# Kernel optimization log

Measured on AMD Instinct MI355X. Metric: run time of the kernel, lower is better.

## Reference

```python
import jax, jax.numpy as jnp
import numpy as np


def setup_inputs() -> dict:
    key = jax.random.key(0)
    k0, k1, k2, k3 = jax.random.split(key, 4)
    T, H, I, E = 2048, 2048, 5632, 8
    return {
        "hidden_states": jax.random.normal(k0, (T, H), dtype=jnp.float32),
        "gate_w": jax.random.normal(k1, (E, H), dtype=jnp.float32) * 0.02,
        "w1": jax.random.normal(k2, (E, 2 * I, H), dtype=jnp.float32) * 0.02,
        "w2": jax.random.normal(k3, (E, H, I), dtype=jnp.float32) * 0.02,
        "top_k": 2,
    }


def reference(hidden_states, gate_w, w1, w2, top_k):
    # hidden_states: [T, H]; gate_w: [E, H]; w1: [E, 2I, H]; w2: [E, H, I]
    T = hidden_states.shape[0]
    E = w1.shape[0]
    router_logits = hidden_states @ gate_w.T                    # [T, E]
    probs = jax.nn.softmax(router_logits, axis=-1)
    topk_w, topk_idx = jax.lax.top_k(probs, top_k)              # [T, k]
    # renormalize=False in fused_moe: use raw softmax top-k weights.
    # Dense combine matrix C[t, e] = weight of expert e for token t (0 if unrouted).
    combine = jnp.zeros((T, E), dtype=probs.dtype)
    combine = combine.at[jnp.arange(T)[:, None], topk_idx].add(topk_w)
    out = jnp.zeros_like(hidden_states)
    for e in range(E):  # small fixed expert loop
        gate_up = hidden_states @ w1[e].T                       # [T, 2I]
        g, u = jnp.split(gate_up, 2, axis=-1)
        h = jax.nn.silu(g) * u                                  # SiluAndMul
        out = out + combine[:, e:e + 1] * (h @ w2[e].T)         # [T, H]
    return out
```

## Files before the change

kernel.cpp:

```cpp
#include <hip/hip_runtime.h>
#include <hip/hip_bf16.h>

typedef __bf16 bf16_t;
typedef __bf16 bf16x8 __attribute__((ext_vector_type(8)));
typedef float  f32x4  __attribute__((ext_vector_type(4)));

constexpr int T_ = 2048, H_ = 2048, I_ = 5632, E_ = 8, S_ = T_ * 2;

constexpr size_t OFF_HB    = 0;
constexpr size_t OFF_HOUT  = OFF_HB    + (size_t)T_ * H_ * 2;
constexpr size_t OFF_DPART = OFF_HOUT  + (size_t)S_ * I_ * 2;
constexpr size_t OFF_TOS   = OFF_DPART + (size_t)S_ * H_ * 4;
constexpr size_t OFF_SOT   = OFF_TOS   + (size_t)S_ * 4;
constexpr size_t OFF_TKI   = OFF_SOT   + (size_t)S_ * 4;
constexpr size_t OFF_TKW   = OFF_TKI   + (size_t)S_ * 4;
constexpr size_t OFF_CNT   = OFF_TKW   + (size_t)S_ * 4;
constexpr size_t OFF_OFFS  = OFF_CNT   + 64;
constexpr size_t OFF_CUR   = OFF_OFFS  + 64;

__device__ __forceinline__ void gload16(const void* g, void* l) {
  __builtin_amdgcn_global_load_lds(
      (const __attribute__((address_space(1))) void*)g,
      (__attribute__((address_space(3))) void*)l, 16, 0, 0);
}

__device__ __forceinline__ bf16x8 cvt8(f32x4 a, f32x4 b) {
  bf16x8 r;
  r[0]=(bf16_t)a[0]; r[1]=(bf16_t)a[1]; r[2]=(bf16_t)a[2]; r[3]=(bf16_t)a[3];
  r[4]=(bf16_t)b[0]; r[5]=(bf16_t)b[1]; r[6]=(bf16_t)b[2]; r[7]=(bf16_t)b[3];
  return r;
}

__global__ __launch_bounds__(256)
void router_kernel(const float* __restrict__ hs, const float* __restrict__ gw,
                   int* __restrict__ tki, float* __restrict__ tkw,
                   int* __restrict__ counts, bf16_t* __restrict__ hb)
{
  const int t = blockIdx.x;
  const int tid = threadIdx.x;
  const int lane = tid & 63, wid = tid >> 6;
  const float* hrow = hs + (size_t)t * H_;
  const int c0 = tid * 8;
  float4 h0 = *(const float4*)(hrow + c0);
  float4 h1 = *(const float4*)(hrow + c0 + 4);
  bf16x8 hv;
  hv[0]=(bf16_t)h0.x; hv[1]=(bf16_t)h0.y; hv[2]=(bf16_t)h0.z; hv[3]=(bf16_t)h0.w;
  hv[4]=(bf16_t)h1.x; hv[5]=(bf16_t)h1.y; hv[6]=(bf16_t)h1.z; hv[7]=(bf16_t)h1.w;
  *(bf16x8*)(hb + (size_t)t * H_ + c0) = hv;

  float acc[E_];
  #pragma unroll
  for (int e = 0; e < E_; ++e) {
    const float* g = gw + (size_t)e * H_ + c0;
    float4 g0 = *(const float4*)(g);
    float4 g1 = *(const float4*)(g + 4);
    acc[e] = h0.x*g0.x + h0.y*g0.y + h0.z*g0.z + h0.w*g0.w
           + h1.x*g1.x + h1.y*g1.y + h1.z*g1.z + h1.w*g1.w;
  }
  #pragma unroll
  for (int e = 0; e < E_; ++e)
    #pragma unroll
    for (int o = 32; o > 0; o >>= 1)
      acc[e] += __shfl_down(acc[e], o);
  __shared__ float red[4][E_];
  if (lane == 0)
    #pragma unroll
    for (int e = 0; e < E_; ++e) red[wid][e] = acc[e];
  __syncthreads();
  if (tid == 0) {
    float l[E_];
    #pragma unroll
    for (int e = 0; e < E_; ++e) l[e] = red[0][e] + red[1][e] + red[2][e] + red[3][e];
    float m = l[0];
    #pragma unroll
    for (int e = 1; e < E_; ++e) m = fmaxf(m, l[e]);
    float p[E_]; float s = 0.f;
    #pragma unroll
    for (int e = 0; e < E_; ++e) { p[e] = __expf(l[e] - m); s += p[e]; }
    int i1 = 0;
    #pragma unroll
    for (int e = 1; e < E_; ++e) if (l[e] > l[i1]) i1 = e;
    int i2 = (i1 == 0) ? 1 : 0;
    #pragma unroll
    for (int e = 0; e < E_; ++e) if (e != i1 && l[e] > l[i2]) i2 = e;
    tki[2*t] = i1; tki[2*t+1] = i2;
    tkw[2*t] = p[i1] / s; tkw[2*t+1] = p[i2] / s;
    atomicAdd(&counts[i1], 1);
    atomicAdd(&counts[i2], 1);
  }
}

__global__ void scan_kernel(const int* __restrict__ counts, const int* __restrict__ tki,
                            int* __restrict__ offs, int* __restrict__ cursor,
                            int* __restrict__ tos, int* __restrict__ sot)
{
  if (threadIdx.x == 0) {
    int run = 0;
    for (int e = 0; e < E_; ++e) { offs[e] = run; cursor[e] = run; run += counts[e]; }
  }
  __syncthreads();
  for (int t = threadIdx.x; t < T_; t += blockDim.x) {
    #pragma unroll
    for (int k = 0; k < 2; ++k) {
      int e = tki[2*t + k];
      int s = atomicAdd(&cursor[e], 1);
      tos[s] = t;
      sot[2*t + k] = s;
    }
  }
}

constexpr int G1_BM = 128, G1_BN = 64, G1_BK = 32;
constexpr int G1_BUF = 8192 + 16384;

__global__ __launch_bounds__(256, 3)
void gemm1_kernel(const bf16_t* __restrict__ hb, const float* __restrict__ w1,
                  const int* __restrict__ tos, const int* __restrict__ offs,
                  const int* __restrict__ counts, bf16_t* __restrict__ hout)
{
  const int bid = blockIdx.x;
  const int e   = bid & 7;
  const int idx = bid >> 3;
  const int mt  = idx & 15;
  const int nt  = idx >> 4;

  const int cnt = counts[e];
  const int m0 = mt * G1_BM;
  if (m0 >= cnt) return;
  const int off = offs[e];
  const int n0 = nt * G1_BN;

  const float* Wg = w1 + (size_t)e * (2 * (size_t)I_ * H_) + (size_t)n0 * H_;

  __shared__ char smem[2 * G1_BUF];

  const int tid = threadIdx.x;
  const int lane = tid & 63, wid = tid >> 6;
  const int wm = wid >> 1, wn = wid & 1;
  const int l15 = lane & 15, l4 = lane >> 4;

  const bf16_t* agp[2]; int aoff[2];
  #pragma unroll
  for (int i = 0; i < 2; ++i) {
    int q = wid * 2 + i;
    int rp = q * 8 + (lane >> 3);
    int w  = (lane & 7) ^ (rp & 7);
    int row = 2 * rp + (w >> 2);
    int slot = off + m0 + row, mx = off + cnt - 1;
    if (slot > mx) slot = mx;
    agp[i]  = hb + (size_t)tos[slot] * H_ + (w & 3) * 8;
    aoff[i] = q * 1024;
  }
  const float* bgp[4]; int boff[4];
  #pragma unroll
  for (int i = 0; i < 4; ++i) {
    int q = wid * 4 + i;
    int row = q * 8 + (lane >> 3);
    int w   = (lane & 7) ^ (row & 7);
    size_t wr = (row < 64) ? (size_t)row : (size_t)(I_ - 64 + row);
    bgp[i]  = Wg + wr * H_ + w * 4;
    boff[i] = q * 1024;
  }

  auto stage = [&](int b, int t) {
    char* ab = smem + b * G1_BUF;
    char* bb = ab + 8192;
    const int k0 = t * G1_BK;
    #pragma unroll
    for (int i = 0; i < 2; ++i) gload16(agp[i] + k0, ab + aoff[i]);
    #pragma unroll
    for (int i = 0; i < 4; ++i) gload16(bgp[i] + k0, bb + boff[i]);
  };

  f32x4 accg[4][2], accu[4][2];
  #pragma unroll
  for (int mi = 0; mi < 4; ++mi)
    #pragma unroll
    for (int ni = 0; ni < 2; ++ni) {
      accg[mi][ni] = f32x4{0.f,0.f,0.f,0.f};
      accu[mi][ni] = f32x4{0.f,0.f,0.f,0.f};
    }

  const int physA = ((((l15 & 1) << 2) | l4) ^ ((l15 >> 1) & 7)) * 16;
  const int aro   = (l15 >> 1);
  const int pB0   = (((2 * l4) ^ (l15 & 7))) * 16;

  auto compute = [&](int b) {
    const char* ab = smem + b * G1_BUF;
    const char* bb = ab + 8192;
    bf16x8 af[4], bgf[2], buf2[2];
    #pragma unroll
    for (int mi = 0; mi < 4; ++mi) {
      int rp = wm * 32 + mi * 8 + aro;
      af[mi] = *(const bf16x8*)(ab + rp * 128 + physA);
    }
    #pragma unroll
    for (int ni = 0; ni < 2; ++ni) {
      int rg = wn * 32 + ni * 16 + l15;
      const char* rowg = bb + rg * 128;
      const char* rowu = bb + (rg + 64) * 128;
      f32x4 g0 = *(const f32x4*)(rowg + pB0);
      f32x4 g1 = *(const f32x4*)(rowg + (pB0 ^ 16));
      f32x4 u0 = *(const f32x4*)(rowu + pB0);
      f32x4 u1 = *(const f32x4*)(rowu + (pB0 ^ 16));
      bgf[ni]  = cvt8(g0, g1);
      buf2[ni] = cvt8(u0, u1);
    }
    #pragma unroll
    for (int mi = 0; mi < 4; ++mi)
      #pragma unroll
      for (int ni = 0; ni < 2; ++ni) {
        accg[mi][ni] = __builtin_amdgcn_mfma_f32_16x16x32_bf16(af[mi], bgf[ni],  accg[mi][ni], 0, 0, 0);
        accu[mi][ni] = __builtin_amdgcn_mfma_f32_16x16x32_bf16(af[mi], buf2[ni], accu[mi][ni], 0, 0, 0);
      }
  };

  constexpr int NK = H_ / G1_BK;
  stage(0, 0);
  __syncthreads();
  int cur = 0;
  for (int t = 0; t < NK; ++t) {
    if (t + 1 < NK) stage(cur ^ 1, t + 1);
    compute(cur);
    __syncthreads();
    cur ^= 1;
  }

  #pragma unroll
  for (int mi = 0; mi < 4; ++mi)
    #pragma unroll
    for (int ni = 0; ni < 2; ++ni)
      #pragma unroll
      for (int j = 0; j < 4; ++j) {
        int rel = wm*64 + mi*16 + l4*4 + j;
        if (m0 + rel < cnt) {
          int col = n0 + wn*32 + ni*16 + l15;
          float g = accg[mi][ni][j];
          float u = accu[mi][ni][j];
          float hvv = (g / (1.0f + __expf(-g))) * u;
          hout[(size_t)(off + m0 + rel) * I_ + col] = (bf16_t)hvv;
        }
      }
}

constexpr int G2_BM = 128, G2_BN = 128, G2_BK = 32;
constexpr int G2_BUF = 8192 + 16384;

__global__ __launch_bounds__(256, 3)
void gemm2_kernel(const bf16_t* __restrict__ hbuf, const float* __restrict__ w2,
                  const int* __restrict__ offs, const int* __restrict__ counts,
                  float* __restrict__ dpart)
{
  const int bid = blockIdx.x;
  const int e   = bid & 7;
  const int idx = bid >> 3;
  const int mt  = idx & 15;
  const int nt  = idx >> 4;

  const int cnt = counts[e];
  const int m0 = mt * G2_BM;
  if (m0 >= cnt) return;
  const int off = offs[e];
  const int n0 = nt * G2_BN;
  const float* W = w2 + (size_t)e * ((size_t)H_ * I_) + (size_t)n0 * I_;

  __shared__ char smem[2 * G2_BUF];

  const int tid = threadIdx.x;
  const int lane = tid & 63, wid = tid >> 6;
  const int wm = wid >> 1, wn = wid & 1;
  const int l15 = lane & 15, l4 = lane >> 4;

  const bf16_t* agp[2]; int aoff[2];
  #pragma unroll
  for (int i = 0; i < 2; ++i) {
    int q = wid * 2 + i;
    int rp = q * 8 + (lane >> 3);
    int w  = (lane & 7) ^ (rp & 7);
    int row = 2 * rp + (w >> 2);
    int slot = off + m0 + row, mx = off + cnt - 1;
    if (slot > mx) slot = mx;
    agp[i]  = hbuf + (size_t)slot * I_ + (w & 3) * 8;
    aoff[i] = q * 1024;
  }
  const float* bgp[4]; int boff[4];
  #pragma unroll
  for (int i = 0; i < 4; ++i) {
    int q = wid * 4 + i;
    int row = q * 8 + (lane >> 3);
    int w   = (lane & 7) ^ (row & 7);
    bgp[i]  = W + (size_t)row * I_ + w * 4;
    boff[i] = q * 1024;
  }

  auto stage = [&](int b, int t) {
    char* ab = smem + b * G2_BUF;
    char* bb = ab + 8192;
    const int k0 = t * G2_BK;
    #pragma unroll
    for (int i = 0; i < 2; ++i) gload16(agp[i] + k0, ab + aoff[i]);
    #pragma unroll
    for (int i = 0; i < 4; ++i) gload16(bgp[i] + k0, bb + boff[i]);
  };

  f32x4 acc[4][4];
  #pragma unroll
  for (int mi = 0; mi < 4; ++mi)
    #pragma unroll
    for (int ni = 0; ni < 4; ++ni) acc[mi][ni] = f32x4{0.f,0.f,0.f,0.f};

  const int physA = ((((l15 & 1) << 2) | l4) ^ ((l15 >> 1) & 7)) * 16;
  const int aro   = (l15 >> 1);
  const int pB0   = (((2 * l4) ^ (l15 & 7))) * 16;

  auto compute = [&](int b) {
    const char* ab = smem + b * G2_BUF;
    const char* bb = ab + 8192;
    bf16x8 af[4], bf[4];
    #pragma unroll
    for (int mi = 0; mi < 4; ++mi) {
      int rp = wm * 32 + mi * 8 + aro;
      af[mi] = *(const bf16x8*)(ab + rp * 128 + physA);
    }
    #pragma unroll
    for (int ni = 0; ni < 4; ++ni) {
      int r = wn * 64 + ni * 16 + l15;
      const char* rowb = bb + r * 128;
      f32x4 b0 = *(const f32x4*)(rowb + pB0);
      f32x4 b1 = *(const f32x4*)(rowb + (pB0 ^ 16));
      bf[ni] = cvt8(b0, b1);
    }
    #pragma unroll
    for (int mi = 0; mi < 4; ++mi)
      #pragma unroll
      for (int ni = 0; ni < 4; ++ni)
        acc[mi][ni] = __builtin_amdgcn_mfma_f32_16x16x32_bf16(af[mi], bf[ni], acc[mi][ni], 0, 0, 0);
  };

  constexpr int NK = I_ / G2_BK;
  stage(0, 0);
  __syncthreads();
  int cur = 0;
  for (int t = 0; t < NK; ++t) {
    if (t + 1 < NK) stage(cur ^ 1, t + 1);
    compute(cur);
    __syncthreads();
    cur ^= 1;
  }

  #pragma unroll
  for (int mi = 0; mi < 4; ++mi)
    #pragma unroll
    for (int ni = 0; ni < 4; ++ni)
      #pragma unroll
      for (int j = 0; j < 4; ++j) {
        int rel = wm*64 + mi*16 + l4*4 + j;
        if (m0 + rel < cnt) {
          int col = n0 + wn*64 + ni*16 + l15;
          dpart[(size_t)(off + m0 + rel) * H_ + col] = acc[mi][ni][j];
        }
      }
}

__global__ __launch_bounds__(256)
void combine_kernel(const float* __restrict__ dpart, const int* __restrict__ sot,
                    const float* __restrict__ tkw, float* __restrict__ out)
{
  int idx = blockIdx.x * 256 + threadIdx.x;
  int t = idx >> 9;
  int c = (idx & 511) * 4;
  float wA = tkw[2*t], wB = tkw[2*t+1];
  int sA = sot[2*t], sB = sot[2*t+1];
  float4 a = *(const float4*)(dpart + (size_t)sA * H_ + c);
  float4 b = *(const float4*)(dpart + (size_t)sB * H_ + c);
  float4 o;
  o.x = wA*a.x + wB*b.x; o.y = wA*a.y + wB*b.y;
  o.z = wA*a.z + wB*b.z; o.w = wA*a.w + wB*b.w;
  *(float4*)(out + (size_t)t * H_ + c) = o;
}

extern "C" void kernel_launch(void* const* d_in, const int* in_sizes, int n_in,
                              void* d_out, int out_size, void* d_ws, size_t ws_size,
                              hipStream_t stream) {
  const float* hs = (const float*)d_in[0];
  const float* gw = (const float*)d_in[1];
  const float* w1 = (const float*)d_in[2];
  const float* w2 = (const float*)d_in[3];
  float* out = (float*)d_out;
  char* ws = (char*)d_ws;

  bf16_t* hb    = (bf16_t*)(ws + OFF_HB);
  bf16_t* hout  = (bf16_t*)(ws + OFF_HOUT);
  float*  dpart = (float*) (ws + OFF_DPART);
  int*    tos   = (int*)   (ws + OFF_TOS);
  int*    sot   = (int*)   (ws + OFF_SOT);
  int*    tki   = (int*)   (ws + OFF_TKI);
  float*  tkw   = (float*) (ws + OFF_TKW);
  int*    cnt   = (int*)   (ws + OFF_CNT);
  int*    offp  = (int*)   (ws + OFF_OFFS);
  int*    curp  = (int*)   (ws + OFF_CUR);

  hipMemsetAsync(ws + OFF_CNT, 0, 64, stream);

  router_kernel<<<T_, 256, 0, stream>>>(hs, gw, tki, tkw, cnt, hb);
  scan_kernel<<<1, 256, 0, stream>>>(cnt, tki, offp, curp, tos, sot);
  gemm1_kernel<<<(T_ / G1_BM) * (I_ / G1_BN) * E_, 256, 0, stream>>>(hb, w1, tos, offp, cnt, hout);
  gemm2_kernel<<<(T_ / G2_BM) * (H_ / G2_BN) * E_, 256, 0, stream>>>(hout, w2, offp, cnt, dpart);
  combine_kernel<<<(T_ * H_ / 4) / 256, 256, 0, stream>>>(dpart, sot, tkw, out);
}
```

Baseline: 905.2 us.

## Retile expert GEMMs to 256-row tiles with 512-thread blocks

Both expert GEMM kernels move from 256-thread blocks with 128-row tiles to 512-thread blocks (8 waves) with 256-row M tiles. Each fp32 weight tile loaded from HBM is therefore reused across twice as many tokens. gemm2's N tile shrinks from 128 to 64, and the swizzle and staging index math is rewritten to match. This cuts weight re-reads, which dominate traffic since the weights are fp32. The cost is fewer, larger blocks, lower occupancy (2 blocks per CU), and more wasted rows on partially filled expert tiles.

```diff
diff --git a/kernel.cpp b/kernel.cpp
--- a/kernel.cpp
+++ b/kernel.cpp
@@ -110,10 +110,9 @@
   }
 }
 
-constexpr int G1_BM = 128, G1_BN = 64, G1_BK = 32;
-constexpr int G1_BUF = 8192 + 16384;
-
-__global__ __launch_bounds__(256, 3)
+constexpr int G1_BUF = 32768;
+
+__global__ __launch_bounds__(512, 2)
 void gemm1_kernel(const bf16_t* __restrict__ hb, const float* __restrict__ w1,
                   const int* __restrict__ tos, const int* __restrict__ offs,
                   const int* __restrict__ counts, bf16_t* __restrict__ hout)
@@ -121,14 +120,14 @@
   const int bid = blockIdx.x;
   const int e   = bid & 7;
   const int idx = bid >> 3;
-  const int mt  = idx & 15;
-  const int nt  = idx >> 4;
+  const int mt  = idx & 7;
+  const int nt  = idx >> 3;
 
   const int cnt = counts[e];
-  const int m0 = mt * G1_BM;
+  const int m0 = mt * 256;
   if (m0 >= cnt) return;
   const int off = offs[e];
-  const int n0 = nt * G1_BN;
+  const int n0 = nt * 64;
 
   const float* Wg = w1 + (size_t)e * (2 * (size_t)I_ * H_) + (size_t)n0 * H_;
 
@@ -143,20 +142,19 @@
   #pragma unroll
   for (int i = 0; i < 2; ++i) {
     int q = wid * 2 + i;
-    int rp = q * 8 + (lane >> 3);
-    int w  = (lane & 7) ^ (rp & 7);
-    int row = 2 * rp + (w >> 2);
+    int w = (lane & 7) ^ (lane >> 3);
+    int row = 2 * (q * 8 + (lane >> 3)) + (w >> 2);
     int slot = off + m0 + row, mx = off + cnt - 1;
     if (slot > mx) slot = mx;
     agp[i]  = hb + (size_t)tos[slot] * H_ + (w & 3) * 8;
     aoff[i] = q * 1024;
   }
-  const float* bgp[4]; int boff[4];
-  #pragma unroll
-  for (int i = 0; i < 4; ++i) {
-    int q = wid * 4 + i;
+  const float* bgp[2]; int boff[2];
+  #pragma unroll
+  for (int i = 0; i < 2; ++i) {
+    int q = wid * 2 + i;
     int row = q * 8 + (lane >> 3);
-    int w   = (lane & 7) ^ (row & 7);
+    int w   = (lane & 7) ^ (lane >> 3);
     size_t wr = (row < 64) ? (size_t)row : (size_t)(I_ - 64 + row);
     bgp[i]  = Wg + wr * H_ + w * 4;
     boff[i] = q * 1024;
@@ -164,12 +162,12 @@
 
   auto stage = [&](int b, int t) {
     char* ab = smem + b * G1_BUF;
-    char* bb = ab + 8192;
-    const int k0 = t * G1_BK;
+    char* bb = ab + 16384;
+    const int k0 = t * 32;
     #pragma unroll
     for (int i = 0; i < 2; ++i) gload16(agp[i] + k0, ab + aoff[i]);
     #pragma unroll
-    for (int i = 0; i < 4; ++i) gload16(bgp[i] + k0, bb + boff[i]);
+    for (int i = 0; i < 2; ++i) gload16(bgp[i] + k0, bb + boff[i]);
   };
 
   f32x4 accg[4][2], accu[4][2];
@@ -182,16 +180,15 @@
     }
 
   const int physA = ((((l15 & 1) << 2) | l4) ^ ((l15 >> 1) & 7)) * 16;
-  const int aro   = (l15 >> 1);
-  const int pB0   = (((2 * l4) ^ (l15 & 7))) * 16;
+  const int pB0   = ((2 * l4) ^ (l15 & 7)) * 16;
 
   auto compute = [&](int b) {
     const char* ab = smem + b * G1_BUF;
-    const char* bb = ab + 8192;
+    const char* bb = ab + 16384;
     bf16x8 af[4], bgf[2], buf2[2];
     #pragma unroll
     for (int mi = 0; mi < 4; ++mi) {
-      int rp = wm * 32 + mi * 8 + aro;
+      int rp = wm * 32 + mi * 8 + (l15 >> 1);
       af[mi] = *(const bf16x8*)(ab + rp * 128 + physA);
     }
     #pragma unroll
@@ -215,7 +212,7 @@
       }
   };
 
-  constexpr int NK = H_ / G1_BK;
+  constexpr int NK = H_ / 32;
   stage(0, 0);
   __syncthreads();
   int cur = 0;
@@ -243,10 +240,9 @@
       }
 }
 
-constexpr int G2_BM = 128, G2_BN = 128, G2_BK = 32;
-constexpr int G2_BUF = 8192 + 16384;
-
-__global__ __launch_bounds__(256, 3)
+constexpr int G2_BUF = 24576;
+
+__global__ __launch_bounds__(512, 2)
 void gemm2_kernel(const bf16_t* __restrict__ hbuf, const float* __restrict__ w2,
                   const int* __restrict__ offs, const int* __restrict__ counts,
                   float* __restrict__ dpart)
@@ -254,14 +250,14 @@
   const int bid = blockIdx.x;
   const int e   = bid & 7;
   const int idx = bid >> 3;
-  const int mt  = idx & 15;
-  const int nt  = idx >> 4;
+  const int mt  = idx & 7;
+  const int nt  = idx >> 3;
 
   const int cnt = counts[e];
-  const int m0 = mt * G2_BM;
+  const int m0 = mt * 256;
   if (m0 >= cnt) return;
   const int off = offs[e];
-  const int n0 = nt * G2_BN;
+  const int n0 = nt * 64;
   const float* W = w2 + (size_t)e * ((size_t)H_ * I_) + (size_t)n0 * I_;
 
   __shared__ char smem[2 * G2_BUF];
@@ -275,56 +271,47 @@
   #pragma unroll
   for (int i = 0; i < 2; ++i) {
     int q = wid * 2 + i;
-    int rp = q * 8 + (lane >> 3);
-    int w  = (lane & 7) ^ (rp & 7);
-    int row = 2 * rp + (w >> 2);
+    int w = (lane & 7) ^ (lane >> 3);
+    int row = 2 * (q * 8 + (lane >> 3)) + (w >> 2);
     int slot = off + m0 + row, mx = off + cnt - 1;
     if (slot > mx) slot = mx;
     agp[i]  = hbuf + (size_t)slot * I_ + (w & 3) * 8;
     aoff[i] = q * 1024;
   }
-  const float* bgp[4]; int boff[4];
-  #pragma unroll
-  for (int i = 0; i < 4; ++i) {
-    int q = wid * 4 + i;
-    int row = q * 8 + (lane >> 3);
-    int w   = (lane & 7) ^ (row & 7);
-    bgp[i]  = W + (size_t)row * I_ + w * 4;
-    boff[i] = q * 1024;
-  }
+  int w_ = (lane & 7) ^ (lane >> 3);
+  const float* bgp = W + (size_t)(wid * 8 + (lane >> 3)) * I_ + w_ * 4;
+  const int boff = wid * 1024;
 
   auto stage = [&](int b, int t) {
     char* ab = smem + b * G2_BUF;
-    char* bb = ab + 8192;
-    const int k0 = t * G2_BK;
+    char* bb = ab + 16384;
+    const int k0 = t * 32;
     #pragma unroll
     for (int i = 0; i < 2; ++i) gload16(agp[i] + k0, ab + aoff[i]);
-    #pragma unroll
-    for (int i = 0; i < 4; ++i) gload16(bgp[i] + k0, bb + boff[i]);
+    gload16(bgp + k0, bb + boff);
   };
 
-  f32x4 acc[4][4];
+  f32x4 acc[4][2];
   #pragma unroll
   for (int mi = 0; mi < 4; ++mi)
     #pragma unroll
-    for (int ni = 0; ni < 4; ++ni) acc[mi][ni] = f32x4{0.f,0.f,0.f,0.f};
+    for (int ni = 0; ni < 2; ++ni) acc[mi][ni] = f32x4{0.f,0.f,0.f,0.f};
 
   const int physA = ((((l15 & 1) << 2) | l4) ^ ((l15 >> 1) & 7)) * 16;
-  const int aro   = (l15 >> 1);
-  const int pB0   = (((2 * l4) ^ (l15 & 7))) * 16;
+  const int pB0   = ((2 * l4) ^ (l15 & 7)) * 16;
 
   auto compute = [&](int b) {
     const char* ab = smem + b * G2_BUF;
-    const char* bb = ab + 8192;
-    bf16x8 af[4], bf[4];
+    const char* bb = ab + 16384;
+    bf16x8 af[4], bf[2];
     #pragma unroll
     for (int mi = 0; mi < 4; ++mi) {
-      int rp = wm * 32 + mi * 8 + aro;
+      int rp = wm * 32 + mi * 8 + (l15 >> 1);
       af[mi] = *(const bf16x8*)(ab + rp * 128 + physA);
     }
     #pragma unroll
-    for (int ni = 0; ni < 4; ++ni) {
-      int r = wn * 64 + ni * 16 + l15;
+    for (int ni = 0; ni < 2; ++ni) {
+      int r = wn * 32 + ni * 16 + l15;
       const char* rowb = bb + r * 128;
       f32x4 b0 = *(const f32x4*)(rowb + pB0);
       f32x4 b1 = *(const f32x4*)(rowb + (pB0 ^ 16));
@@ -333,11 +320,11 @@
     #pragma unroll
     for (int mi = 0; mi < 4; ++mi)
       #pragma unroll
-      for (int ni = 0; ni < 4; ++ni)
+      for (int ni = 0; ni < 2; ++ni)
         acc[mi][ni] = __builtin_amdgcn_mfma_f32_16x16x32_bf16(af[mi], bf[ni], acc[mi][ni], 0, 0, 0);
   };
 
-  constexpr int NK = I_ / G2_BK;
+  constexpr int NK = I_ / 32;
   stage(0, 0);
   __syncthreads();
   int cur = 0;
@@ -351,12 +338,12 @@
   #pragma unroll
   for (int mi = 0; mi < 4; ++mi)
     #pragma unroll
-    for (int ni = 0; ni < 4; ++ni)
+    for (int ni = 0; ni < 2; ++ni)
       #pragma unroll
       for (int j = 0; j < 4; ++j) {
         int rel = wm*64 + mi*16 + l4*4 + j;
         if (m0 + rel < cnt) {
-          int col = n0 + wn*64 + ni*16 + l15;
+          int col = n0 + wn*32 + ni*16 + l15;
           dpart[(size_t)(off + m0 + rel) * H_ + col] = acc[mi][ni][j];
         }
       }
@@ -404,7 +391,7 @@
 
   router_kernel<<<T_, 256, 0, stream>>>(hs, gw, tki, tkw, cnt, hb);
   scan_kernel<<<1, 256, 0, stream>>>(cnt, tki, offp, curp, tos, sot);
-  gemm1_kernel<<<(T_ / G1_BM) * (I_ / G1_BN) * E_, 256, 0, stream>>>(hb, w1, tos, offp, cnt, hout);
-  gemm2_kernel<<<(T_ / G2_BM) * (H_ / G2_BN) * E_, 256, 0, stream>>>(hout, w2, offp, cnt, dpart);
+  gemm1_kernel<<<8 * (2 * I_ / 128) * E_, 512, 0, stream>>>(hb, w1, tos, offp, cnt, hout);
+  gemm2_kernel<<<8 * (H_ / 64) * E_, 512, 0, stream>>>(hout, w2, offp, cnt, dpart);
   combine_kernel<<<(T_ * H_ / 4) / 256, 256, 0, stream>>>(dpart, sot, tkw, out);
 }
```

Result: slower. 1.128 ms (+24.6%).

## Load fp32 weight fragments directly to registers, bypassing LDS for B operand

Applied to the files above, without the earlier changes.

Both expert GEMMs stop staging the fp32 weight tile through shared memory. Each lane now reads its MFMA B fragment straight from global memory into registers one step ahead and converts it to bf16 after the MFMAs run. Only the bf16 activation tile stays in LDS, using a smaller 64-byte-row swizzle. This cuts the LDS footprint and LDS traffic, which may allow higher occupancy, but weight reuse across the two M-waves now depends on the cache and each lane issues more global loads.

```diff
diff --git a/kernel.cpp b/kernel.cpp
--- a/kernel.cpp
+++ b/kernel.cpp
@@ -110,8 +110,7 @@
   }
 }
 
-constexpr int G1_BM = 128, G1_BN = 64, G1_BK = 32;
-constexpr int G1_BUF = 8192 + 16384;
+constexpr int G1_BUF = 8192;
 
 __global__ __launch_bounds__(256, 3)
 void gemm1_kernel(const bf16_t* __restrict__ hb, const float* __restrict__ w1,
@@ -125,10 +124,10 @@
   const int nt  = idx >> 4;
 
   const int cnt = counts[e];
-  const int m0 = mt * G1_BM;
+  const int m0 = mt * 128;
   if (m0 >= cnt) return;
   const int off = offs[e];
-  const int n0 = nt * G1_BN;
+  const int n0 = nt * 64;
 
   const float* Wg = w1 + (size_t)e * (2 * (size_t)I_ * H_) + (size_t)n0 * H_;
 
@@ -143,33 +142,35 @@
   #pragma unroll
   for (int i = 0; i < 2; ++i) {
     int q = wid * 2 + i;
-    int rp = q * 8 + (lane >> 3);
-    int w  = (lane & 7) ^ (rp & 7);
-    int row = 2 * rp + (w >> 2);
-    int slot = off + m0 + row, mx = off + cnt - 1;
+    int R = q * 16 + (lane >> 2);
+    int wanted = (lane & 3) ^ ((lane >> 2) & 3);
+    int slot = off + m0 + R, mx = off + cnt - 1;
     if (slot > mx) slot = mx;
-    agp[i]  = hb + (size_t)tos[slot] * H_ + (w & 3) * 8;
+    agp[i]  = hb + (size_t)tos[slot] * H_ + wanted * 8;
     aoff[i] = q * 1024;
   }
-  const float* bgp[4]; int boff[4];
-  #pragma unroll
-  for (int i = 0; i < 4; ++i) {
-    int q = wid * 4 + i;
-    int row = q * 8 + (lane >> 3);
-    int w   = (lane & 7) ^ (row & 7);
-    size_t wr = (row < 64) ? (size_t)row : (size_t)(I_ - 64 + row);
-    bgp[i]  = Wg + wr * H_ + w * 4;
-    boff[i] = q * 1024;
-  }
-
-  auto stage = [&](int b, int t) {
+  auto stageA = [&](int b, int t) {
     char* ab = smem + b * G1_BUF;
-    char* bb = ab + 8192;
-    const int k0 = t * G1_BK;
-    #pragma unroll
-    for (int i = 0; i < 2; ++i) gload16(agp[i] + k0, ab + aoff[i]);
-    #pragma unroll
-    for (int i = 0; i < 4; ++i) gload16(bgp[i] + k0, bb + boff[i]);
+    #pragma unroll
+    for (int i = 0; i < 2; ++i) gload16(agp[i] + t * 32, ab + aoff[i]);
+  };
+
+  const float* bp00 = Wg + (size_t)(wn * 32 +  0 + l15) * H_ + l4 * 8;
+  const float* bp01 = Wg + (size_t)(wn * 32 + 16 + l15) * H_ + l4 * 8;
+  const float* bp10 = bp00 + (size_t)I_ * H_;
+  const float* bp11 = bp01 + (size_t)I_ * H_;
+
+  f32x4 br0, br1, br2, br3, br4, br5, br6, br7;
+  auto loadB = [&](int k0) {
+    br0 = *(const f32x4*)(bp00 + k0); br1 = *(const f32x4*)(bp00 + k0 + 4);
+    br2 = *(const f32x4*)(bp01 + k0); br3 = *(const f32x4*)(bp01 + k0 + 4);
+    br4 = *(const f32x4*)(bp10 + k0); br5 = *(const f32x4*)(bp10 + k0 + 4);
+    br6 = *(const f32x4*)(bp11 + k0); br7 = *(const f32x4*)(bp11 + k0 + 4);
+  };
+  bf16x8 bgf0, bgf1, buf0, buf1;
+  auto cvtB = [&]() {
+    bgf0 = cvt8(br0, br1); bgf1 = cvt8(br2, br3);
+    buf0 = cvt8(br4, br5); buf1 = cvt8(br6, br7);
   };
 
   f32x4 accg[4][2], accu[4][2];
@@ -181,47 +182,33 @@
       accu[mi][ni] = f32x4{0.f,0.f,0.f,0.f};
     }
 
-  const int physA = ((((l15 & 1) << 2) | l4) ^ ((l15 >> 1) & 7)) * 16;
-  const int aro   = (l15 >> 1);
-  const int pB0   = (((2 * l4) ^ (l15 & 7))) * 16;
-
+  const int achunk = (l4 ^ (l15 & 3)) * 16;
   auto compute = [&](int b) {
     const char* ab = smem + b * G1_BUF;
-    const char* bb = ab + 8192;
-    bf16x8 af[4], bgf[2], buf2[2];
+    bf16x8 af[4];
     #pragma unroll
     for (int mi = 0; mi < 4; ++mi) {
-      int rp = wm * 32 + mi * 8 + aro;
-      af[mi] = *(const bf16x8*)(ab + rp * 128 + physA);
-    }
-    #pragma unroll
-    for (int ni = 0; ni < 2; ++ni) {
-      int rg = wn * 32 + ni * 16 + l15;
-      const char* rowg = bb + rg * 128;
-      const char* rowu = bb + (rg + 64) * 128;
-      f32x4 g0 = *(const f32x4*)(rowg + pB0);
-      f32x4 g1 = *(const f32x4*)(rowg + (pB0 ^ 16));
-      f32x4 u0 = *(const f32x4*)(rowu + pB0);
-      f32x4 u1 = *(const f32x4*)(rowu + (pB0 ^ 16));
-      bgf[ni]  = cvt8(g0, g1);
-      buf2[ni] = cvt8(u0, u1);
-    }
-    #pragma unroll
-    for (int mi = 0; mi < 4; ++mi)
-      #pragma unroll
-      for (int ni = 0; ni < 2; ++ni) {
-        accg[mi][ni] = __builtin_amdgcn_mfma_f32_16x16x32_bf16(af[mi], bgf[ni],  accg[mi][ni], 0, 0, 0);
-        accu[mi][ni] = __builtin_amdgcn_mfma_f32_16x16x32_bf16(af[mi], buf2[ni], accu[mi][ni], 0, 0, 0);
-      }
-  };
-
-  constexpr int NK = H_ / G1_BK;
-  stage(0, 0);
+      int R = wm * 64 + mi * 16 + l15;
+      af[mi] = *(const bf16x8*)(ab + R * 64 + achunk);
+    }
+    #pragma unroll
+    for (int mi = 0; mi < 4; ++mi) {
+      accg[mi][0] = __builtin_amdgcn_mfma_f32_16x16x32_bf16(af[mi], bgf0, accg[mi][0], 0, 0, 0);
+      accg[mi][1] = __builtin_amdgcn_mfma_f32_16x16x32_bf16(af[mi], bgf1, accg[mi][1], 0, 0, 0);
+      accu[mi][0] = __builtin_amdgcn_mfma_f32_16x16x32_bf16(af[mi], buf0, accu[mi][0], 0, 0, 0);
+      accu[mi][1] = __builtin_amdgcn_mfma_f32_16x16x32_bf16(af[mi], buf1, accu[mi][1], 0, 0, 0);
+    }
+  };
+
+  constexpr int NK = H_ / 32;
+  loadB(0); stageA(0, 0);
+  cvtB();
   __syncthreads();
   int cur = 0;
   for (int t = 0; t < NK; ++t) {
-    if (t + 1 < NK) stage(cur ^ 1, t + 1);
+    if (t + 1 < NK) { loadB((t + 1) * 32); stageA(cur ^ 1, t + 1); }
     compute(cur);
+    if (t + 1 < NK) cvtB();
     __syncthreads();
     cur ^= 1;
   }
@@ -243,8 +230,7 @@
       }
 }
 
-constexpr int G2_BM = 128, G2_BN = 128, G2_BK = 32;
-constexpr int G2_BUF = 8192 + 16384;
+constexpr int G2_BUF = 8192;
 
 __global__ __launch_bounds__(256, 3)
 void gemm2_kernel(const bf16_t* __restrict__ hbuf, const float* __restrict__ w2,
@@ -258,10 +244,10 @@
   const int nt  = idx >> 4;
 
   const int cnt = counts[e];
-  const int m0 = mt * G2_BM;
+  const int m0 = mt * 128;
   if (m0 >= cnt) return;
   const int off = offs[e];
-  const int n0 = nt * G2_BN;
+  const int n0 = nt * 128;
   const float* W = w2 + (size_t)e * ((size_t)H_ * I_) + (size_t)n0 * I_;
 
   __shared__ char smem[2 * G2_BUF];
@@ -275,32 +261,35 @@
   #pragma unroll
   for (int i = 0; i < 2; ++i) {
     int q = wid * 2 + i;
-    int rp = q * 8 + (lane >> 3);
-    int w  = (lane & 7) ^ (rp & 7);
-    int row = 2 * rp + (w >> 2);
-    int slot = off + m0 + row, mx = off + cnt - 1;
+    int R = q * 16 + (lane >> 2);
+    int wanted = (lane & 3) ^ ((lane >> 2) & 3);
+    int slot = off + m0 + R, mx = off + cnt - 1;
     if (slot > mx) slot = mx;
-    agp[i]  = hbuf + (size_t)slot * I_ + (w & 3) * 8;
+    agp[i]  = hbuf + (size_t)slot * I_ + wanted * 8;
     aoff[i] = q * 1024;
   }
-  const float* bgp[4]; int boff[4];
-  #pragma unroll
-  for (int i = 0; i < 4; ++i) {
-    int q = wid * 4 + i;
-    int row = q * 8 + (lane >> 3);
-    int w   = (lane & 7) ^ (row & 7);
-    bgp[i]  = W + (size_t)row * I_ + w * 4;
-    boff[i] = q * 1024;
-  }
-
-  auto stage = [&](int b, int t) {
+  auto stageA = [&](int b, int t) {
     char* ab = smem + b * G2_BUF;
-    char* bb = ab + 8192;
-    const int k0 = t * G2_BK;
-    #pragma unroll
-    for (int i = 0; i < 2; ++i) gload16(agp[i] + k0, ab + aoff[i]);
-    #pragma unroll
-    for (int i = 0; i < 4; ++i) gload16(bgp[i] + k0, bb + boff[i]);
+    #pragma unroll
+    for (int i = 0; i < 2; ++i) gload16(agp[i] + t * 32, ab + aoff[i]);
+  };
+
+  const float* bp0 = W + (size_t)(wn * 64 +  0 + l15) * I_ + l4 * 8;
+  const float* bp1 = W + (size_t)(wn * 64 + 16 + l15) * I_ + l4 * 8;
+  const float* bp2 = W + (size_t)(wn * 64 + 32 + l15) * I_ + l4 * 8;
+  const float* bp3 = W + (size_t)(wn * 64 + 48 + l15) * I_ + l4 * 8;
+
+  f32x4 br0, br1, br2, br3, br4, br5, br6, br7;
+  auto loadB = [&](int k0) {
+    br0 = *(const f32x4*)(bp0 + k0); br1 = *(const f32x4*)(bp0 + k0 + 4);
+    br2 = *(const f32x4*)(bp1 + k0); br3 = *(const f32x4*)(bp1 + k0 + 4);
+    br4 = *(const f32x4*)(bp2 + k0); br5 = *(const f32x4*)(bp2 + k0 + 4);
+    br6 = *(const f32x4*)(bp3 + k0); br7 = *(const f32x4*)(bp3 + k0 + 4);
+  };
+  bf16x8 bf0, bf1, bf2, bf3;
+  auto cvtB = [&]() {
+    bf0 = cvt8(br0, br1); bf1 = cvt8(br2, br3);
+    bf2 = cvt8(br4, br5); bf3 = cvt8(br6, br7);
   };
 
   f32x4 acc[4][4];
@@ -309,41 +298,33 @@
     #pragma unroll
     for (int ni = 0; ni < 4; ++ni) acc[mi][ni] = f32x4{0.f,0.f,0.f,0.f};
 
-  const int physA = ((((l15 & 1) << 2) | l4) ^ ((l15 >> 1) & 7)) * 16;
-  const int aro   = (l15 >> 1);
-  const int pB0   = (((2 * l4) ^ (l15 & 7))) * 16;
-
+  const int achunk = (l4 ^ (l15 & 3)) * 16;
   auto compute = [&](int b) {
     const char* ab = smem + b * G2_BUF;
-    const char* bb = ab + 8192;
-    bf16x8 af[4], bf[4];
+    bf16x8 af[4];
     #pragma unroll
     for (int mi = 0; mi < 4; ++mi) {
-      int rp = wm * 32 + mi * 8 + aro;
-      af[mi] = *(const bf16x8*)(ab + rp * 128 + physA);
-    }
-    #pragma unroll
-    for (int ni = 0; ni < 4; ++ni) {
-      int r = wn * 64 + ni * 16 + l15;
-      const char* rowb = bb + r * 128;
-      f32x4 b0 = *(const f32x4*)(rowb + pB0);
-      f32x4 b1 = *(const f32x4*)(rowb + (pB0 ^ 16));
-      bf[ni] = cvt8(b0, b1);
-    }
-    #pragma unroll
-    for (int mi = 0; mi < 4; ++mi)
-      #pragma unroll
-      for (int ni = 0; ni < 4; ++ni)
-        acc[mi][ni] = __builtin_amdgcn_mfma_f32_16x16x32_bf16(af[mi], bf[ni], acc[mi][ni], 0, 0, 0);
-  };
-
-  constexpr int NK = I_ / G2_BK;
-  stage(0, 0);
+      int R = wm * 64 + mi * 16 + l15;
+      af[mi] = *(const bf16x8*)(ab + R * 64 + achunk);
+    }
+    #pragma unroll
+    for (int mi = 0; mi < 4; ++mi) {
+      acc[mi][0] = __builtin_amdgcn_mfma_f32_16x16x32_bf16(af[mi], bf0, acc[mi][0], 0, 0, 0);
+      acc[mi][1] = __builtin_amdgcn_mfma_f32_16x16x32_bf16(af[mi], bf1, acc[mi][1], 0, 0, 0);
+      acc[mi][2] = __builtin_amdgcn_mfma_f32_16x16x32_bf16(af[mi], bf2, acc[mi][2], 0, 0, 0);
+      acc[mi][3] = __builtin_amdgcn_mfma_f32_16x16x32_bf16(af[mi], bf3, acc[mi][3], 0, 0, 0);
+    }
+  };
+
+  constexpr int NK = I_ / 32;
+  loadB(0); stageA(0, 0);
+  cvtB();
   __syncthreads();
   int cur = 0;
   for (int t = 0; t < NK; ++t) {
-    if (t + 1 < NK) stage(cur ^ 1, t + 1);
+    if (t + 1 < NK) { loadB((t + 1) * 32); stageA(cur ^ 1, t + 1); }
     compute(cur);
+    if (t + 1 < NK) cvtB();
     __syncthreads();
     cur ^= 1;
   }
@@ -404,7 +385,7 @@
 
   router_kernel<<<T_, 256, 0, stream>>>(hs, gw, tki, tkw, cnt, hb);
   scan_kernel<<<1, 256, 0, stream>>>(cnt, tki, offp, curp, tos, sot);
-  gemm1_kernel<<<(T_ / G1_BM) * (I_ / G1_BN) * E_, 256, 0, stream>>>(hb, w1, tos, offp, cnt, hout);
-  gemm2_kernel<<<(T_ / G2_BM) * (H_ / G2_BN) * E_, 256, 0, stream>>>(hout, w2, offp, cnt, dpart);
+  gemm1_kernel<<<16 * (2 * I_ / 128) * E_ / 8 * 8, 256, 0, stream>>>(hb, w1, tos, offp, cnt, hout);
+  gemm2_kernel<<<16 * (H_ / 128) * E_, 256, 0, stream>>>(hout, w2, offp, cnt, dpart);
   combine_kernel<<<(T_ * H_ / 4) / 256, 256, 0, stream>>>(dpart, sot, tkw, out);
 }
```

Measured after the change: 2.204 ms. +143.5%, slower.
